# Performance work log

Hardware: AMD Instinct MI355X
Metric: run time of the kernel (lower is better)

Reference implementation:

```python
import jax, jax.numpy as jnp
import numpy as np

N, E, G, H, IN = 200000, 400000, 64, 128, 5
LN_EPS = 1e-5


def setup_inputs() -> dict:
    key = jax.random.key(0)
    ks = jax.random.split(key, 32)
    d = {}
    d["x"] = jax.random.normal(ks[0], (N, IN), jnp.float32)
    d["edge_index"] = jax.random.randint(ks[1], (2, E), 0, N, dtype=jnp.int32)
    d["edge_attr"] = jax.random.normal(ks[2], (E, 1), jnp.float32)
    d["batch"] = jnp.sort(jax.random.randint(ks[3], (N,), 0, G, dtype=jnp.int32))
    dims = [IN, H, H]
    i = 4
    names = [("ew", "eb", "w1_", "b1_", "w2_", "b2_", "g", "bt")]
    for l, din in enumerate(dims):
        d[f"ew{l}"] = jax.random.normal(ks[i], (1, din), jnp.float32); i += 1
        d[f"eb{l}"] = jnp.zeros((din,), jnp.float32)
        d[f"w1_{l}"] = jax.random.normal(ks[i], (din, H), jnp.float32) / np.sqrt(din); i += 1
        d[f"b1_{l}"] = jnp.zeros((H,), jnp.float32)
        d[f"w2_{l}"] = jax.random.normal(ks[i], (H, H), jnp.float32) / np.sqrt(H); i += 1
        d[f"b2_{l}"] = jnp.zeros((H,), jnp.float32)
        d[f"g{l}"] = jnp.ones((H,), jnp.float32)
        d[f"bt{l}"] = jnp.zeros((H,), jnp.float32)
    return d


def _gine_layer(x, src, dst, edge_attr, ew, eb, w1, b1, w2, b2, g, bt):
    # edge encoder: Linear(1, din)
    e = edge_attr @ ew + eb                       # [E, din]
    # GINEConv message: ReLU(x_j + e), aggregated (sum) at destination
    m = jax.nn.relu(x[src] + e)                   # [E, din]
    aggr = jax.ops.segment_sum(m, dst, num_segments=N)  # [N, din]
    h = x + aggr                                  # (1 + eps)*x with eps=0
    # GIN MLP: Linear -> ReLU -> Linear
    h = jax.nn.relu(h @ w1 + b1) @ w2 + b2        # [N, H]
    # LayerNorm
    mu = jnp.mean(h, axis=-1, keepdims=True)
    var = jnp.mean((h - mu) ** 2, axis=-1, keepdims=True)
    h = (h - mu) * jax.lax.rsqrt(var + LN_EPS) * g + bt
    return jax.nn.relu(h)


def reference(x, edge_index, edge_attr, batch,
              ew0, eb0, w1_0, b1_0, w2_0, b2_0, g0, bt0,
              ew1, eb1, w1_1, b1_1, w2_1, b2_1, g1, bt1,
              ew2, eb2, w1_2, b1_2, w2_2, b2_2, g2, bt2):
    src, dst = edge_index[0], edge_index[1]
    x = _gine_layer(x, src, dst, edge_attr, ew0, eb0, w1_0, b1_0, w2_0, b2_0, g0, bt0)
    x = _gine_layer(x, src, dst, edge_attr, ew1, eb1, w1_1, b1_1, w2_1, b2_1, g1, bt1)
    x = _gine_layer(x, src, dst, edge_attr, ew2, eb2, w1_2, b1_2, w2_2, b2_2, g2, bt2)
    # global pooling per graph
    add_pool = jax.ops.segment_sum(x, batch, num_segments=G)           # [G, H]
    counts = jax.ops.segment_sum(jnp.ones((N,), x.dtype), batch, num_segments=G)
    mean_pool = add_pool / jnp.maximum(counts, 1.0)[:, None]           # [G, H]
    return jnp.concatenate([mean_pool, add_pool], axis=1)              # [G, 2H]
```

## Files before the change

### kernel.cpp

```cpp
#include <hip/hip_runtime.h>

#define N_NODES 200000
#define N_EDGES 400000
#define N_GRAPHS 64
#define HDIM 128
#define INDIM 5
#define LN_EPS 1e-5f
#define LDA 140
#define NPBLK 64

typedef __attribute__((ext_vector_type(8))) short short8;
typedef __attribute__((ext_vector_type(4))) float f32x4;
typedef __attribute__((ext_vector_type(2))) float f32x2;

__device__ __forceinline__ unsigned short to_bf(float v) {
    unsigned u = __builtin_bit_cast(unsigned, v);
    return (unsigned short)((u + 0x7FFFu + ((u >> 16) & 1u)) >> 16);
}
__device__ __forceinline__ float bf_lo(unsigned w) { return __builtin_bit_cast(float, w << 16); }
__device__ __forceinline__ float bf_hi(unsigned w) { return __builtin_bit_cast(float, w & 0xFFFF0000u); }
__device__ __forceinline__ float bf2f(unsigned short h) { return __builtin_bit_cast(float, (unsigned)h << 16); }

__device__ __forceinline__ unsigned short cvt1_bf(float v) {
    unsigned r;
    asm("v_cvt_pk_bf16_f32 %0, %1, %1" : "=v"(r) : "v"(v));
    return (unsigned short)r;
}
__device__ __forceinline__ unsigned cvt2_bf(float lo, float hi) {
    unsigned r;
    asm("v_cvt_pk_bf16_f32 %0, %1, %2" : "=v"(r) : "v"(lo), "v"(hi));
    return r;
}
__device__ __forceinline__ f32x2 vmax0(f32x2 v) {
#if __has_builtin(__builtin_elementwise_max)
    return __builtin_elementwise_max(v, (f32x2)0.f);
#else
    v.x = fmaxf(v.x, 0.f);
    v.y = fmaxf(v.y, 0.f);
    return v;
#endif
}

#define GLOAD(p0, p1, p2, p3, srcrow)                                       \
    {                                                                       \
        const uint4* xs_ = (const uint4*)(xin + (size_t)(srcrow)*128 + c0); \
        p0 = xs_[0]; p1 = xs_[1]; p2 = xs_[2]; p3 = xs_[3];                 \
    }

#define GP2(wd, i0)            \
    {                          \
        float4 wb_ = ep[i0];   \
        f32x2 xv_;             \
        xv_.x = bf_lo(wd);     \
        xv_.y = bf_hi(wd);     \
        f32x2 ew_, eb_;        \
        ew_.x = wb_.x;         \
        ew_.y = wb_.y;         \
        eb_.x = wb_.z;         \
        eb_.y = wb_.w;         \
        f32x2 t_ = xv_ + eb_;  \
        t_ = av2_ * ew_ + t_;  \
        accv[i0] += vmax0(t_); \
    }

#define GPROC(p0, p1, p2, p3, a_)                               \
    {                                                           \
        f32x2 av2_;                                             \
        av2_.x = (a_);                                          \
        av2_.y = (a_);                                          \
        GP2(p0.x, 0) GP2(p0.y, 1) GP2(p0.z, 2) GP2(p0.w, 3)     \
        GP2(p1.x, 4) GP2(p1.y, 5) GP2(p1.z, 6) GP2(p1.w, 7)     \
        GP2(p2.x, 8) GP2(p2.y, 9) GP2(p2.z, 10) GP2(p2.w, 11)   \
        GP2(p3.x, 12) GP2(p3.y, 13) GP2(p3.z, 14) GP2(p3.w, 15) \
    }

#define GI2(wd, i0)             \
    {                           \
        accv[i0].x = bf_lo(wd); \
        accv[i0].y = bf_hi(wd); \
    }

#define GINIT(p0, p1, p2, p3)                                   \
    {                                                           \
        GI2(p0.x, 0) GI2(p0.y, 1) GI2(p0.z, 2) GI2(p0.w, 3)     \
        GI2(p1.x, 4) GI2(p1.y, 5) GI2(p1.z, 6) GI2(p1.w, 7)     \
        GI2(p2.x, 8) GI2(p2.y, 9) GI2(p2.z, 10) GI2(p2.w, 11)   \
        GI2(p3.x, 12) GI2(p3.y, 13) GI2(p3.z, 14) GI2(p3.w, 15) \
    }


__global__ void hist_kernel(const int* __restrict__ ei, int* __restrict__ deg) {
    int e = blockIdx.x * blockDim.x + threadIdx.x;
    if (e < N_EDGES) atomicAdd(&deg[ei[N_EDGES + e]], 1);
}

#define SCAN_CHUNK 1024
#define SCAN_BLOCKS ((N_NODES + SCAN_CHUNK - 1) / SCAN_CHUNK)

__global__ __launch_bounds__(256) void scan_phaseA(const int* __restrict__ deg, int* __restrict__ bsums,
                                                   int* __restrict__ poolz) {
    if (blockIdx.x == 0) {
        for (int i = threadIdx.x; i < N_GRAPHS * HDIM + N_GRAPHS; i += 256) poolz[i] = 0;
    }
    __shared__ int red[256];
    int t = threadIdx.x;
    int base = blockIdx.x * SCAN_CHUNK + t * 4;
    int s = 0;
#pragma unroll
    for (int k = 0; k < 4; ++k) {
        int i = base + k;
        s += (i < N_NODES) ? deg[i] : 0;
    }
    red[t] = s;
    __syncthreads();
    for (int off = 128; off; off >>= 1) {
        if (t < off) red[t] += red[t + off];
        __syncthreads();
    }
    if (t == 0) bsums[blockIdx.x] = red[0];
}

__global__ __launch_bounds__(256) void scan_phaseB(int* __restrict__ bsums, int* __restrict__ row_ptr) {
    __shared__ int s[256];
    int t = threadIdx.x;
    int v = (t < SCAN_BLOCKS) ? bsums[t] : 0;
    s[t] = v;
    __syncthreads();
    for (int off = 1; off < 256; off <<= 1) {
        int add = (t >= off) ? s[t - off] : 0;
        __syncthreads();
        s[t] += add;
        __syncthreads();
    }
    if (t < SCAN_BLOCKS) bsums[t] = s[t] - v;
    if (t == SCAN_BLOCKS - 1) row_ptr[N_NODES] = s[t];
}

__global__ __launch_bounds__(256) void scan_phaseC(const int* __restrict__ deg,
                                                   const int* __restrict__ bsums,
                                                   int* __restrict__ row_ptr,
                                                   int* __restrict__ cursor) {
    __shared__ int ts[256];
    int t = threadIdx.x;
    int base = blockIdx.x * SCAN_CHUNK + t * 4;
    int v[4];
    int s = 0;
#pragma unroll
    for (int k = 0; k < 4; ++k) {
        int i = base + k;
        v[k] = (i < N_NODES) ? deg[i] : 0;
        s += v[k];
    }
    ts[t] = s;
    __syncthreads();
    for (int off = 1; off < 256; off <<= 1) {
        int add = (t >= off) ? ts[t - off] : 0;
        __syncthreads();
        ts[t] += add;
        __syncthreads();
    }
    int run = bsums[blockIdx.x] + ts[t] - s;
#pragma unroll
    for (int k = 0; k < 4; ++k) {
        int i = base + k;
        if (i < N_NODES) { row_ptr[i] = run; cursor[i] = 0; }
        run += v[k];
    }
}

#define SCATTER_BLOCKS ((N_EDGES + 255) / 256)

__global__ void scatter_pack(const int* __restrict__ ei, const float* __restrict__ ea,
                             const int* __restrict__ row_ptr, int* __restrict__ cursor,
                             int2* __restrict__ csr,
                             const float* __restrict__ s0, short* __restrict__ d0,
                             const float* __restrict__ s1, short* __restrict__ d1,
                             const float* __restrict__ s2, short* __restrict__ d2,
                             const float* __restrict__ s3, short* __restrict__ d3,
                             const float* __restrict__ s4, short* __restrict__ d4,
                             const float* __restrict__ s5, short* __restrict__ d5) {
    int b = blockIdx.x;
    if (b < SCATTER_BLOCKS) {
        int e = b * 256 + threadIdx.x;
        if (e >= N_EDGES) return;
        int d = ei[N_EDGES + e];
        int pos = atomicAdd(&cursor[d], 1);
        csr[row_ptr[d] + pos] = make_int2(ei[e], __float_as_int(ea[e]));
        return;
    }
    b -= SCATTER_BLOCKS;
    const float* W;
    short* D;
    int din, KP, b0;
    if (b < 16)       { W = s0; D = d0; din = 5;   KP = 32;  b0 = 0; }
    else if (b < 80)  { W = s1; D = d1; din = 128; KP = 128; b0 = 16; }
    else if (b < 144) { W = s2; D = d2; din = 128; KP = 128; b0 = 80; }
    else if (b < 208) { W = s3; D = d3; din = 128; KP = 128; b0 = 144; }
    else if (b < 272) { W = s4; D = d4; din = 128; KP = 128; b0 = 208; }
    else              { W = s5; D = d5; din = 128; KP = 128; b0 = 272; }
    int idx = (b - b0) * 256 + threadIdx.x;
    if (idx >= KP * 128) return;
    int j = idx & 7;
    int lane = (idx >> 3) & 63;
    int rest = idx >> 9;
    int KS = KP >> 5;
    int kstep = rest % KS;
    int tile = rest / KS;
    int k = kstep * 32 + ((lane >> 4) * 8) + j;
    int n = tile * 16 + (lane & 15);
    float v = (k < din) ? W[k * 128 + n] : 0.f;
    D[idx] = (short)to_bf(v);
}

template <int KP1, bool POOL>
__global__ __launch_bounds__(256, 4) void layer_fused(
    const void* __restrict__ xin_v, const int* __restrict__ row_ptr,
    const int2* __restrict__ csr,
    const float* __restrict__ ew, const float* __restrict__ eb,
    const short* __restrict__ w1h, const float* __restrict__ b1,
    const short* __restrict__ w2h, const float* __restrict__ b2,
    const float* __restrict__ g, const float* __restrict__ bt,
    unsigned short* __restrict__ xout,
    const int* __restrict__ batch, float* __restrict__ pool, int* __restrict__ cnt) {
    __shared__ __align__(16) unsigned short A16[NPBLK * LDA];
    __shared__ int bidx[NPBLK];
    union Scratch {
        float4 eweb4[4 * 17];
        float part[KP1 == 128 ? 1 : NPBLK][4][INDIM];
    };
    __shared__ __align__(16) Scratch u;

    int tid = threadIdx.x;
    int node0 = blockIdx.x * NPBLK;

    if constexpr (KP1 == 128) {
        const unsigned short* xin = (const unsigned short*)xin_v;
        if (tid < 64) {
            int qq = tid >> 4, ii = tid & 15, c = qq * 32 + ii * 2;
            u.eweb4[qq * 17 + ii] = make_float4(ew[c], ew[c + 1], eb[c], eb[c + 1]);
        }
        if (POOL && tid >= 64 && tid < 128) bidx[tid - 64] = batch[node0 + tid - 64];

        int row = tid >> 2, qt = tid & 3, c0 = qt * 32;
        int node = node0 + row;

        const uint4* xn = (const uint4*)(xin + (size_t)node * 128 + c0);
        uint4 o0 = xn[0], o1 = xn[1], o2 = xn[2], o3 = xn[3];
        int beg = row_ptr[node], end = row_ptr[node + 1];

        uint4 va0, va1, va2, va3;
        float aA = 0.f;
        int2 rC = make_int2(0, 0), rD = rC;
        if (beg < end) {
            int2 r = csr[beg];
            aA = __int_as_float(r.y);
            GLOAD(va0, va1, va2, va3, r.x);
        }
        if (beg + 1 < end) rC = csr[beg + 1];
        if (beg + 2 < end) rD = csr[beg + 2];
        __syncthreads();
        const float4* ep = u.eweb4 + qt * 17;

        f32x2 accv[16];
        GINIT(o0, o1, o2, o3);

        int e = beg;
        while (e + 1 < end) {
            GPROC(va0, va1, va2, va3, aA);
            aA = __int_as_float(rC.y);
            GLOAD(va0, va1, va2, va3, rC.x);
            rC = rD;
            int i3 = min(e + 3, end - 1);
            rD = csr[i3];
            ++e;
        }
        if (e < end) GPROC(va0, va1, va2, va3, aA);

        uint2* Ar2 = (uint2*)&A16[row * LDA + c0];
#pragma unroll
        for (int k = 0; k < 8; ++k) {
            Ar2[k] = make_uint2(cvt2_bf(accv[2 * k].x, accv[2 * k].y),
                                cvt2_bf(accv[2 * k + 1].x, accv[2 * k + 1].y));
        }
    } else {
        const float* xinf = (const float*)xin_v;
        int row = tid >> 2, qt = tid & 3;
        int node = node0 + row;
        {
            float w[INDIM], b[INDIM], acc[INDIM];
#pragma unroll
            for (int j = 0; j < INDIM; ++j) {
                w[j] = ew[j];
                b[j] = eb[j];
                acc[j] = 0.f;
            }
            int beg = row_ptr[node], end = row_ptr[node + 1];
            int2 r;
            if (beg + qt < end) r = csr[beg + qt];
            for (int e = beg + qt; e < end; e += 4) {
                int2 rn = (e + 4 < end) ? csr[e + 4] : r;
                float a = __int_as_float(r.y);
#pragma unroll
                for (int j = 0; j < INDIM; ++j)
                    acc[j] += fmaxf(fmaf(a, w[j], xinf[r.x * INDIM + j] + b[j]), 0.f);
                r = rn;
            }
#pragma unroll
            for (int j = 0; j < INDIM; ++j) u.part[row][qt][j] = acc[j];
        }
        __syncthreads();
        if (tid < NPBLK) {
#pragma unroll
            for (int j = 0; j < INDIM; ++j) {
                float v = xinf[(node0 + tid) * INDIM + j] + u.part[tid][0][j] + u.part[tid][1][j] +
                          u.part[tid][2][j] + u.part[tid][3][j];
                A16[tid * LDA + j] = cvt1_bf(v);
            }
#pragma unroll
            for (int j = INDIM; j < 32; ++j) A16[tid * LDA + j] = 0;
        }
        __syncthreads();
    }

    int wv = tid >> 6, lane = tid & 63;
    int mrow = lane & 15, q = lane >> 4;
    int arow = wv * 16 + mrow;

    const short8* w1p = (const short8*)w1h;
    const short8* w2p = (const short8*)w2h;

    f32x4 acc2[8];
#pragma unroll
    for (int t = 0; t < 8; ++t) acc2[t] = (f32x4){0.f, 0.f, 0.f, 0.f};
    constexpr int KS1 = KP1 / 32;
#pragma unroll
    for (int ks = 0; ks < KS1; ++ks) {
        short8 bh[8];
#pragma unroll
        for (int t = 0; t < 8; ++t) bh[t] = w1p[((size_t)t * KS1 + ks) * 64 + lane];
        short8 ah = *(const short8*)&A16[arow * LDA + ks * 32 + q * 8];
#pragma unroll
        for (int t = 0; t < 8; ++t)
            acc2[t] = __builtin_amdgcn_mfma_f32_16x16x32_bf16(ah, bh[t], acc2[t], 0, 0, 0);
    }
    {
        float b1v[8];
#pragma unroll
        for (int t = 0; t < 8; ++t) b1v[t] = b1[t * 16 + mrow];
#pragma unroll
        for (int t = 0; t < 8; ++t)
#pragma unroll
            for (int r = 0; r < 4; ++r) {
                int rrow = wv * 16 + q * 4 + r;
                int col = t * 16 + mrow;
                A16[rrow * LDA + col] = cvt1_bf(fmaxf(acc2[t][r] + b1v[t], 0.f));
            }
    }

#pragma unroll
    for (int t = 0; t < 8; ++t) acc2[t] = (f32x4){0.f, 0.f, 0.f, 0.f};
#pragma unroll
    for (int ks = 0; ks < 4; ++ks) {
        short8 bh[8];
#pragma unroll
        for (int t = 0; t < 8; ++t) bh[t] = w2p[((size_t)t * 4 + ks) * 64 + lane];
        short8 ah = *(const short8*)&A16[arow * LDA + ks * 32 + q * 8];
#pragma unroll
        for (int t = 0; t < 8; ++t)
            acc2[t] = __builtin_amdgcn_mfma_f32_16x16x32_bf16(ah, bh[t], acc2[t], 0, 0, 0);
    }

    float s4[4] = {0.f, 0.f, 0.f, 0.f}, q4[4] = {0.f, 0.f, 0.f, 0.f};
    {
        float b2v[8];
#pragma unroll
        for (int t = 0; t < 8; ++t) b2v[t] = b2[t * 16 + mrow];
#pragma unroll
        for (int t = 0; t < 8; ++t)
#pragma unroll
            for (int r = 0; r < 4; ++r) {
                float v = acc2[t][r] + b2v[t];
                acc2[t][r] = v;
                s4[r] += v;
                q4[r] += v * v;
            }
    }
#pragma unroll
    for (int m = 1; m <= 8; m <<= 1) {
#pragma unroll
        for (int r = 0; r < 4; ++r) {
            s4[r] += __shfl_xor(s4[r], m, 64);
            q4[r] += __shfl_xor(q4[r], m, 64);
        }
    }
    float mu[4], inv[4];
#pragma unroll
    for (int r = 0; r < 4; ++r) {
        mu[r] = s4[r] * (1.f / HDIM);
        float var = q4[r] * (1.f / HDIM) - mu[r] * mu[r];
        inv[r] = rsqrtf(var + LN_EPS);
    }
    float gv[8], btv[8];
#pragma unroll
    for (int t = 0; t < 8; ++t) {
        gv[t] = g[t * 16 + mrow];
        btv[t] = bt[t * 16 + mrow];
    }

#pragma unroll
    for (int t = 0; t < 8; ++t)
#pragma unroll
        for (int r = 0; r < 4; ++r) {
            int rrow = wv * 16 + q * 4 + r;
            int col = t * 16 + mrow;
            float o = fmaxf((acc2[t][r] - mu[r]) * inv[r] * gv[t] + btv[t], 0.f);
            A16[rrow * LDA + col] = cvt1_bf(o);
        }
    __syncthreads();

    if (!POOL) {
        unsigned* xo = (unsigned*)xout;
#pragma unroll
        for (int i = 0; i < 16; ++i) {
            int idx = tid + 256 * i;
            int row = idx >> 6, w = idx & 63;
            xo[(size_t)(node0 + row) * 64 + w] = ((const unsigned*)&A16[row * LDA])[w];
        }
    } else {
        if (tid < 128) {
            int col = tid;
            float accp = 0.f;
            int cur = bidx[0];
            for (int r = 0; r < NPBLK; ++r) {
                int gi = bidx[r];
                if (gi != cur) {
                    unsafeAtomicAdd(&pool[cur * HDIM + col], accp);
                    accp = 0.f;
                    cur = gi;
                }
                accp += bf2f(A16[r * LDA + col]);
            }
            unsafeAtomicAdd(&pool[cur * HDIM + col], accp);
        } else if (tid == 255) {
            int cur = bidx[0], c = 0;
            for (int r = 0; r < NPBLK; ++r) {
                if (bidx[r] != cur) {
                    atomicAdd(&cnt[cur], c);
                    c = 0;
                    cur = bidx[r];
                }
                ++c;
            }
            atomicAdd(&cnt[cur], c);
        }
    }
}

__global__ void pool_final(const float* __restrict__ pool, const int* __restrict__ cnt,
                           float* __restrict__ out) {
    int g = blockIdx.x, j = threadIdx.x;
    float add = pool[g * HDIM + j];
    float c = (float)max(cnt[g], 1);
    out[g * (2 * HDIM) + j] = add / c;
    out[g * (2 * HDIM) + HDIM + j] = add;
}

extern "C" void kernel_launch(void* const* d_in, const int* in_sizes, int n_in,
                              void* d_out, int out_size, void* d_ws, size_t ws_size,
                              hipStream_t stream) {
    const float* x_in = (const float*)d_in[0];
    const int* ei = (const int*)d_in[1];
    const float* ea = (const float*)d_in[2];
    const int* batch = (const int*)d_in[3];
    const float* P[24];
    for (int i = 0; i < 24; ++i) P[i] = (const float*)d_in[4 + i];

    unsigned short* x_a = (unsigned short*)d_ws;
    unsigned short* x_b = x_a + (size_t)N_NODES * HDIM;
    float* pool = (float*)(x_b + (size_t)N_NODES * HDIM);
    int* cnt = (int*)(pool + N_GRAPHS * HDIM);
    int* deg = cnt + N_GRAPHS;
    int* cursor = deg + N_NODES;
    int* row_ptr = cursor + N_NODES;
    int* bsums = row_ptr + N_NODES + 1;
    int2* csr = (int2*)(bsums + 256);
    short* wp = (short*)(((uintptr_t)(csr + N_EDGES) + 15) & ~(uintptr_t)15);
    float* out = (float*)d_out;

    short *w1h[3], *w2h[3];
    for (int l = 0; l < 3; ++l) {
        w1h[l] = wp + (size_t)l * 32768;
        w2h[l] = w1h[l] + 16384;
    }

    hipMemsetAsync(deg, 0, N_NODES * sizeof(int), stream);

    hist_kernel<<<(N_EDGES + 255) / 256, 256, 0, stream>>>(ei, deg);
    scan_phaseA<<<SCAN_BLOCKS, 256, 0, stream>>>(deg, bsums, (int*)pool);
    scan_phaseB<<<1, 256, 0, stream>>>(bsums, row_ptr);
    scan_phaseC<<<SCAN_BLOCKS, 256, 0, stream>>>(deg, bsums, row_ptr, cursor);

    scatter_pack<<<SCATTER_BLOCKS + 336, 256, 0, stream>>>(
        ei, ea, row_ptr, cursor, csr,
        P[2], w1h[0], P[4], w2h[0],
        P[10], w1h[1], P[12], w2h[1],
        P[18], w1h[2], P[20], w2h[2]);

    layer_fused<32, false><<<N_NODES / NPBLK, 256, 0, stream>>>(
        x_in, row_ptr, csr, P[0], P[1],
        w1h[0], P[3], w2h[0], P[5], P[6], P[7], x_a, nullptr, nullptr, nullptr);
    layer_fused<128, false><<<N_NODES / NPBLK, 256, 0, stream>>>(
        x_a, row_ptr, csr, P[8], P[9],
        w1h[1], P[11], w2h[1], P[13], P[14], P[15], x_b, nullptr, nullptr, nullptr);
    layer_fused<128, true><<<N_NODES / NPBLK, 256, 0, stream>>>(
        x_b, row_ptr, csr, P[16], P[17],
        w1h[2], P[19], w2h[2], P[21], P[22], P[23], nullptr, batch, pool, cnt);

    pool_final<<<N_GRAPHS, HDIM, 0, stream>>>(pool, cnt, out);
}
```

Measured before the change: 344.2 us.

## Double nodes per block to 128 with two MFMA row tiles per wave

```diff
diff --git a/kernel.cpp b/kernel.cpp
--- a/kernel.cpp
+++ b/kernel.cpp
@@ -7,7 +7,8 @@
 #define INDIM 5
 #define LN_EPS 1e-5f
 #define LDA 140
-#define NPBLK 64
+#define NPBLK 128
+#define NBLKS ((N_NODES + NPBLK - 1) / NPBLK)
 
 typedef __attribute__((ext_vector_type(8))) short short8;
 typedef __attribute__((ext_vector_type(4))) float f32x4;
@@ -41,10 +42,11 @@
 #endif
 }
 
-#define GLOAD(p0, p1, p2, p3, srcrow)                                       \
+#define GLOAD8(y0, y1, y2, y3, y4, y5, y6, y7, srcrow)                      \
     {                                                                       \
         const uint4* xs_ = (const uint4*)(xin + (size_t)(srcrow)*128 + c0); \
-        p0 = xs_[0]; p1 = xs_[1]; p2 = xs_[2]; p3 = xs_[3];                 \
+        y0 = xs_[0]; y1 = xs_[1]; y2 = xs_[2]; y3 = xs_[3];                 \
+        y4 = xs_[4]; y5 = xs_[5]; y6 = xs_[6]; y7 = xs_[7];                 \
     }
 
 #define GP2(wd, i0)            \
@@ -63,15 +65,19 @@
         accv[i0] += vmax0(t_); \
     }
 
-#define GPROC(p0, p1, p2, p3, a_)                               \
+#define GPROC8(y0, y1, y2, y3, y4, y5, y6, y7, a_)              \
     {                                                           \
         f32x2 av2_;                                             \
         av2_.x = (a_);                                          \
         av2_.y = (a_);                                          \
-        GP2(p0.x, 0) GP2(p0.y, 1) GP2(p0.z, 2) GP2(p0.w, 3)     \
-        GP2(p1.x, 4) GP2(p1.y, 5) GP2(p1.z, 6) GP2(p1.w, 7)     \
-        GP2(p2.x, 8) GP2(p2.y, 9) GP2(p2.z, 10) GP2(p2.w, 11)   \
-        GP2(p3.x, 12) GP2(p3.y, 13) GP2(p3.z, 14) GP2(p3.w, 15) \
+        GP2(y0.x, 0) GP2(y0.y, 1) GP2(y0.z, 2) GP2(y0.w, 3)     \
+        GP2(y1.x, 4) GP2(y1.y, 5) GP2(y1.z, 6) GP2(y1.w, 7)     \
+        GP2(y2.x, 8) GP2(y2.y, 9) GP2(y2.z, 10) GP2(y2.w, 11)   \
+        GP2(y3.x, 12) GP2(y3.y, 13) GP2(y3.z, 14) GP2(y3.w, 15) \
+        GP2(y4.x, 16) GP2(y4.y, 17) GP2(y4.z, 18) GP2(y4.w, 19) \
+        GP2(y5.x, 20) GP2(y5.y, 21) GP2(y5.z, 22) GP2(y5.w, 23) \
+        GP2(y6.x, 24) GP2(y6.y, 25) GP2(y6.z, 26) GP2(y6.w, 27) \
+        GP2(y7.x, 28) GP2(y7.y, 29) GP2(y7.z, 30) GP2(y7.w, 31) \
     }
 
 #define GI2(wd, i0)             \
@@ -80,12 +86,16 @@
         accv[i0].y = bf_hi(wd); \
     }
 
-#define GINIT(p0, p1, p2, p3)                                   \
+#define GINIT8(y0, y1, y2, y3, y4, y5, y6, y7)                  \
     {                                                           \
-        GI2(p0.x, 0) GI2(p0.y, 1) GI2(p0.z, 2) GI2(p0.w, 3)     \
-        GI2(p1.x, 4) GI2(p1.y, 5) GI2(p1.z, 6) GI2(p1.w, 7)     \
-        GI2(p2.x, 8) GI2(p2.y, 9) GI2(p2.z, 10) GI2(p2.w, 11)   \
-        GI2(p3.x, 12) GI2(p3.y, 13) GI2(p3.z, 14) GI2(p3.w, 15) \
+        GI2(y0.x, 0) GI2(y0.y, 1) GI2(y0.z, 2) GI2(y0.w, 3)     \
+        GI2(y1.x, 4) GI2(y1.y, 5) GI2(y1.z, 6) GI2(y1.w, 7)     \
+        GI2(y2.x, 8) GI2(y2.y, 9) GI2(y2.z, 10) GI2(y2.w, 11)   \
+        GI2(y3.x, 12) GI2(y3.y, 13) GI2(y3.z, 14) GI2(y3.w, 15) \
+        GI2(y4.x, 16) GI2(y4.y, 17) GI2(y4.z, 18) GI2(y4.w, 19) \
+        GI2(y5.x, 20) GI2(y5.y, 21) GI2(y5.z, 22) GI2(y5.w, 23) \
+        GI2(y6.x, 24) GI2(y6.y, 25) GI2(y6.z, 26) GI2(y6.w, 27) \
+        GI2(y7.x, 28) GI2(y7.y, 29) GI2(y7.z, 30) GI2(y7.w, 31) \
     }
 
 
@@ -225,8 +235,8 @@
     __shared__ __align__(16) unsigned short A16[NPBLK * LDA];
     __shared__ int bidx[NPBLK];
     union Scratch {
-        float4 eweb4[4 * 17];
-        float part[KP1 == 128 ? 1 : NPBLK][4][INDIM];
+        float4 eweb4[2 * 33];
+        float part[KP1 == 128 ? 1 : NPBLK][2][INDIM];
     };
     __shared__ __align__(16) Scratch u;
 
@@ -236,56 +246,57 @@
     if constexpr (KP1 == 128) {
         const unsigned short* xin = (const unsigned short*)xin_v;
         if (tid < 64) {
-            int qq = tid >> 4, ii = tid & 15, c = qq * 32 + ii * 2;
-            u.eweb4[qq * 17 + ii] = make_float4(ew[c], ew[c + 1], eb[c], eb[c + 1]);
-        }
-        if (POOL && tid >= 64 && tid < 128) bidx[tid - 64] = batch[node0 + tid - 64];
-
-        int row = tid >> 2, qt = tid & 3, c0 = qt * 32;
-        int node = node0 + row;
+            int hh = tid >> 5, ii = tid & 31, c = hh * 64 + ii * 2;
+            u.eweb4[hh * 33 + ii] = make_float4(ew[c], ew[c + 1], eb[c], eb[c + 1]);
+        }
+        if (POOL && tid >= 128) bidx[tid - 128] = batch[min(node0 + tid - 128, N_NODES - 1)];
+
+        int row = tid >> 1, half = tid & 1, c0 = half * 64;
+        int node = min(node0 + row, N_NODES - 1);
 
         const uint4* xn = (const uint4*)(xin + (size_t)node * 128 + c0);
         uint4 o0 = xn[0], o1 = xn[1], o2 = xn[2], o3 = xn[3];
+        uint4 o4 = xn[4], o5 = xn[5], o6 = xn[6], o7 = xn[7];
         int beg = row_ptr[node], end = row_ptr[node + 1];
 
-        uint4 va0, va1, va2, va3;
+        uint4 va0, va1, va2, va3, va4, va5, va6, va7;
         float aA = 0.f;
         int2 rC = make_int2(0, 0), rD = rC;
         if (beg < end) {
             int2 r = csr[beg];
             aA = __int_as_float(r.y);
-            GLOAD(va0, va1, va2, va3, r.x);
+            GLOAD8(va0, va1, va2, va3, va4, va5, va6, va7, r.x);
         }
         if (beg + 1 < end) rC = csr[beg + 1];
         if (beg + 2 < end) rD = csr[beg + 2];
         __syncthreads();
-        const float4* ep = u.eweb4 + qt * 17;
-
-        f32x2 accv[16];
-        GINIT(o0, o1, o2, o3);
+        const float4* ep = u.eweb4 + half * 33;
+
+        f32x2 accv[32];
+        GINIT8(o0, o1, o2, o3, o4, o5, o6, o7);
 
         int e = beg;
         while (e + 1 < end) {
-            GPROC(va0, va1, va2, va3, aA);
+            GPROC8(va0, va1, va2, va3, va4, va5, va6, va7, aA);
             aA = __int_as_float(rC.y);
-            GLOAD(va0, va1, va2, va3, rC.x);
+            GLOAD8(va0, va1, va2, va3, va4, va5, va6, va7, rC.x);
             rC = rD;
             int i3 = min(e + 3, end - 1);
             rD = csr[i3];
             ++e;
         }
-        if (e < end) GPROC(va0, va1, va2, va3, aA);
+        if (e < end) GPROC8(va0, va1, va2, va3, va4, va5, va6, va7, aA);
 
         uint2* Ar2 = (uint2*)&A16[row * LDA + c0];
 #pragma unroll
-        for (int k = 0; k < 8; ++k) {
+        for (int k = 0; k < 16; ++k) {
             Ar2[k] = make_uint2(cvt2_bf(accv[2 * k].x, accv[2 * k].y),
                                 cvt2_bf(accv[2 * k + 1].x, accv[2 * k + 1].y));
         }
     } else {
         const float* xinf = (const float*)xin_v;
-        int row = tid >> 2, qt = tid & 3;
-        int node = node0 + row;
+        int row = tid >> 1, qt = tid & 1;
+        int node = min(node0 + row, N_NODES - 1);
         {
             float w[INDIM], b[INDIM], acc[INDIM];
 #pragma unroll
@@ -297,8 +308,8 @@
             int beg = row_ptr[node], end = row_ptr[node + 1];
             int2 r;
             if (beg + qt < end) r = csr[beg + qt];
-            for (int e = beg + qt; e < end; e += 4) {
-                int2 rn = (e + 4 < end) ? csr[e + 4] : r;
+            for (int e = beg + qt; e < end; e += 2) {
+                int2 rn = (e + 2 < end) ? csr[e + 2] : r;
                 float a = __int_as_float(r.y);
 #pragma unroll
                 for (int j = 0; j < INDIM; ++j)
@@ -310,10 +321,10 @@
         }
         __syncthreads();
         if (tid < NPBLK) {
+            int nd = min(node0 + tid, N_NODES - 1);
 #pragma unroll
             for (int j = 0; j < INDIM; ++j) {
-                float v = xinf[(node0 + tid) * INDIM + j] + u.part[tid][0][j] + u.part[tid][1][j] +
-                          u.part[tid][2][j] + u.part[tid][3][j];
+                float v = xinf[nd * INDIM + j] + u.part[tid][0][j] + u.part[tid][1][j];
                 A16[tid * LDA + j] = cvt1_bf(v);
             }
 #pragma unroll
@@ -324,82 +335,105 @@
 
     int wv = tid >> 6, lane = tid & 63;
     int mrow = lane & 15, q = lane >> 4;
-    int arow = wv * 16 + mrow;
+    int ar0 = wv * 32 + mrow;
+    int ar1 = wv * 32 + 16 + mrow;
 
     const short8* w1p = (const short8*)w1h;
     const short8* w2p = (const short8*)w2h;
 
-    f32x4 acc2[8];
-#pragma unroll
-    for (int t = 0; t < 8; ++t) acc2[t] = (f32x4){0.f, 0.f, 0.f, 0.f};
+    f32x4 acc2[2][8];
+#pragma unroll
+    for (int gg = 0; gg < 2; ++gg)
+#pragma unroll
+        for (int t = 0; t < 8; ++t) acc2[gg][t] = (f32x4){0.f, 0.f, 0.f, 0.f};
     constexpr int KS1 = KP1 / 32;
 #pragma unroll
     for (int ks = 0; ks < KS1; ++ks) {
         short8 bh[8];
 #pragma unroll
         for (int t = 0; t < 8; ++t) bh[t] = w1p[((size_t)t * KS1 + ks) * 64 + lane];
-        short8 ah = *(const short8*)&A16[arow * LDA + ks * 32 + q * 8];
-#pragma unroll
-        for (int t = 0; t < 8; ++t)
-            acc2[t] = __builtin_amdgcn_mfma_f32_16x16x32_bf16(ah, bh[t], acc2[t], 0, 0, 0);
+        short8 ah0 = *(const short8*)&A16[ar0 * LDA + ks * 32 + q * 8];
+        short8 ah1 = *(const short8*)&A16[ar1 * LDA + ks * 32 + q * 8];
+#pragma unroll
+        for (int t = 0; t < 8; ++t) {
+            acc2[0][t] = __builtin_amdgcn_mfma_f32_16x16x32_bf16(ah0, bh[t], acc2[0][t], 0, 0, 0);
+            acc2[1][t] = __builtin_amdgcn_mfma_f32_16x16x32_bf16(ah1, bh[t], acc2[1][t], 0, 0, 0);
+        }
     }
     {
         float b1v[8];
 #pragma unroll
         for (int t = 0; t < 8; ++t) b1v[t] = b1[t * 16 + mrow];
 #pragma unroll
-        for (int t = 0; t < 8; ++t)
-#pragma unroll
-            for (int r = 0; r < 4; ++r) {
-                int rrow = wv * 16 + q * 4 + r;
-                int col = t * 16 + mrow;
-                A16[rrow * LDA + col] = cvt1_bf(fmaxf(acc2[t][r] + b1v[t], 0.f));
-            }
-    }
-
-#pragma unroll
-    for (int t = 0; t < 8; ++t) acc2[t] = (f32x4){0.f, 0.f, 0.f, 0.f};
+        for (int gg = 0; gg < 2; ++gg)
+#pragma unroll
+            for (int t = 0; t < 8; ++t)
+#pragma unroll
+                for (int r = 0; r < 4; ++r) {
+                    int rrow = wv * 32 + gg * 16 + q * 4 + r;
+                    int col = t * 16 + mrow;
+                    A16[rrow * LDA + col] = cvt1_bf(fmaxf(acc2[gg][t][r] + b1v[t], 0.f));
+                }
+    }
+
+#pragma unroll
+    for (int gg = 0; gg < 2; ++gg)
+#pragma unroll
+        for (int t = 0; t < 8; ++t) acc2[gg][t] = (f32x4){0.f, 0.f, 0.f, 0.f};
 #pragma unroll
     for (int ks = 0; ks < 4; ++ks) {
         short8 bh[8];
 #pragma unroll
         for (int t = 0; t < 8; ++t) bh[t] = w2p[((size_t)t * 4 + ks) * 64 + lane];
-        short8 ah = *(const short8*)&A16[arow * LDA + ks * 32 + q * 8];
-#pragma unroll
-        for (int t = 0; t < 8; ++t)
-            acc2[t] = __builtin_amdgcn_mfma_f32_16x16x32_bf16(ah, bh[t], acc2[t], 0, 0, 0);
-    }
-
-    float s4[4] = {0.f, 0.f, 0.f, 0.f}, q4[4] = {0.f, 0.f, 0.f, 0.f};
+        short8 ah0 = *(const short8*)&A16[ar0 * LDA + ks * 32 + q * 8];
+        short8 ah1 = *(const short8*)&A16[ar1 * LDA + ks * 32 + q * 8];
+#pragma unroll
+        for (int t = 0; t < 8; ++t) {
+            acc2[0][t] = __builtin_amdgcn_mfma_f32_16x16x32_bf16(ah0, bh[t], acc2[0][t], 0, 0, 0);
+            acc2[1][t] = __builtin_amdgcn_mfma_f32_16x16x32_bf16(ah1, bh[t], acc2[1][t], 0, 0, 0);
+        }
+    }
+
+    float s4[2][4], q4[2][4];
+#pragma unroll
+    for (int gg = 0; gg < 2; ++gg)
+#pragma unroll
+        for (int r = 0; r < 4; ++r) { s4[gg][r] = 0.f; q4[gg][r] = 0.f; }
     {
         float b2v[8];
 #pragma unroll
         for (int t = 0; t < 8; ++t) b2v[t] = b2[t * 16 + mrow];
 #pragma unroll
-        for (int t = 0; t < 8; ++t)
+        for (int gg = 0; gg < 2; ++gg)
+#pragma unroll
+            for (int t = 0; t < 8; ++t)
+#pragma unroll
+                for (int r = 0; r < 4; ++r) {
+                    float v = acc2[gg][t][r] + b2v[t];
+                    acc2[gg][t][r] = v;
+                    s4[gg][r] += v;
+                    q4[gg][r] += v * v;
+                }
+    }
+#pragma unroll
+    for (int m = 1; m <= 8; m <<= 1) {
+#pragma unroll
+        for (int gg = 0; gg < 2; ++gg)
 #pragma unroll
             for (int r = 0; r < 4; ++r) {
-                float v = acc2[t][r] + b2v[t];
-                acc2[t][r] = v;
-                s4[r] += v;
-                q4[r] += v * v;
-            }
-    }
-#pragma unroll
-    for (int m = 1; m <= 8; m <<= 1) {
+                s4[gg][r] += __shfl_xor(s4[gg][r], m, 64);
+                q4[gg][r] += __shfl_xor(q4[gg][r], m, 64);
+            }
+    }
+    float mu[2][4], inv[2][4];
+#pragma unroll
+    for (int gg = 0; gg < 2; ++gg)
 #pragma unroll
         for (int r = 0; r < 4; ++r) {
-            s4[r] += __shfl_xor(s4[r], m, 64);
-            q4[r] += __shfl_xor(q4[r], m, 64);
-        }
-    }
-    float mu[4], inv[4];
-#pragma unroll
-    for (int r = 0; r < 4; ++r) {
-        mu[r] = s4[r] * (1.f / HDIM);
-        float var = q4[r] * (1.f / HDIM) - mu[r] * mu[r];
-        inv[r] = rsqrtf(var + LN_EPS);
-    }
+            mu[gg][r] = s4[gg][r] * (1.f / HDIM);
+            float var = q4[gg][r] * (1.f / HDIM) - mu[gg][r] * mu[gg][r];
+            inv[gg][r] = rsqrtf(var + LN_EPS);
+        }
     float gv[8], btv[8];
 #pragma unroll
     for (int t = 0; t < 8; ++t) {
@@ -408,30 +442,34 @@
     }
 
 #pragma unroll
-    for (int t = 0; t < 8; ++t)
-#pragma unroll
-        for (int r = 0; r < 4; ++r) {
-            int rrow = wv * 16 + q * 4 + r;
-            int col = t * 16 + mrow;
-            float o = fmaxf((acc2[t][r] - mu[r]) * inv[r] * gv[t] + btv[t], 0.f);
-            A16[rrow * LDA + col] = cvt1_bf(o);
-        }
+    for (int gg = 0; gg < 2; ++gg)
+#pragma unroll
+        for (int t = 0; t < 8; ++t)
+#pragma unroll
+            for (int r = 0; r < 4; ++r) {
+                int rrow = wv * 32 + gg * 16 + q * 4 + r;
+                int col = t * 16 + mrow;
+                float o = fmaxf((acc2[gg][t][r] - mu[gg][r]) * inv[gg][r] * gv[t] + btv[t], 0.f);
+                A16[rrow * LDA + col] = cvt1_bf(o);
+            }
     __syncthreads();
 
     if (!POOL) {
         unsigned* xo = (unsigned*)xout;
 #pragma unroll
-        for (int i = 0; i < 16; ++i) {
+        for (int i = 0; i < 32; ++i) {
             int idx = tid + 256 * i;
             int row = idx >> 6, w = idx & 63;
-            xo[(size_t)(node0 + row) * 64 + w] = ((const unsigned*)&A16[row * LDA])[w];
+            if (node0 + row < N_NODES)
+                xo[(size_t)(node0 + row) * 64 + w] = ((const unsigned*)&A16[row * LDA])[w];
         }
     } else {
+        int rmax = min(NPBLK, N_NODES - node0);
         if (tid < 128) {
             int col = tid;
             float accp = 0.f;
             int cur = bidx[0];
-            for (int r = 0; r < NPBLK; ++r) {
+            for (int r = 0; r < rmax; ++r) {
                 int gi = bidx[r];
                 if (gi != cur) {
                     unsafeAtomicAdd(&pool[cur * HDIM + col], accp);
@@ -443,7 +481,7 @@
             unsafeAtomicAdd(&pool[cur * HDIM + col], accp);
         } else if (tid == 255) {
             int cur = bidx[0], c = 0;
-            for (int r = 0; r < NPBLK; ++r) {
+            for (int r = 0; r < rmax; ++r) {
                 if (bidx[r] != cur) {
                     atomicAdd(&cnt[cur], c);
                     c = 0;
@@ -506,13 +544,13 @@
         P[10], w1h[1], P[12], w2h[1],
         P[18], w1h[2], P[20], w2h[2]);
 
-    layer_fused<32, false><<<N_NODES / NPBLK, 256, 0, stream>>>(
+    layer_fused<32, false><<<NBLKS, 256, 0, stream>>>(
         x_in, row_ptr, csr, P[0], P[1],
         w1h[0], P[3], w2h[0], P[5], P[6], P[7], x_a, nullptr, nullptr, nullptr);
-    layer_fused<128, false><<<N_NODES / NPBLK, 256, 0, stream>>>(
+    layer_fused<128, false><<<NBLKS, 256, 0, stream>>>(
         x_a, row_ptr, csr, P[8], P[9],
         w1h[1], P[11], w2h[1], P[13], P[14], P[15], x_b, nullptr, nullptr, nullptr);
-    layer_fused<128, true><<<N_NODES / NPBLK, 256, 0, stream>>>(
+    layer_fused<128, true><<<NBLKS, 256, 0, stream>>>(
         x_b, row_ptr, csr, P[16], P[17],
         w1h[2], P[19], w2h[2], P[21], P[22], P[23], nullptr, batch, pool, cnt);
 
```

Result: slower. 668.4 us (+94.2%).

## Reorder nodes by in-degree within each graph to balance aggregation work

Applied to the files above, without the earlier changes.

```diff
diff --git a/kernel.cpp b/kernel.cpp
--- a/kernel.cpp
+++ b/kernel.cpp
@@ -94,6 +94,58 @@
     if (e < N_EDGES) atomicAdd(&deg[ei[N_EDGES + e]], 1);
 }
 
+__global__ void gbounds(const int* __restrict__ batch, int* __restrict__ gbnd) {
+    int g = threadIdx.x;
+    if (g > N_GRAPHS) return;
+    int lo = 0, hi = N_NODES;
+    while (lo < hi) {
+        int mid = (lo + hi) >> 1;
+        if (batch[mid] < g) lo = mid + 1;
+        else hi = mid;
+    }
+    gbnd[g] = lo;
+}
+
+__global__ __launch_bounds__(256) void gsort(const int* __restrict__ deg,
+                                             const int* __restrict__ gbnd,
+                                             int* __restrict__ perm, int* __restrict__ iperm) {
+    __shared__ int bins[64], offs[64];
+    int g = blockIdx.x;
+    int s = gbnd[g], e2 = gbnd[g + 1];
+    int t = threadIdx.x;
+    if (t < 64) bins[t] = 0;
+    __syncthreads();
+    for (int i = s + t; i < e2; i += 256) atomicAdd(&bins[min(deg[i], 63)], 1);
+    __syncthreads();
+    if (t == 0) {
+        int run = 0;
+        for (int b = 0; b < 64; ++b) { offs[b] = run; run += bins[b]; }
+    }
+    __syncthreads();
+    if (t < 64) bins[t] = 0;
+    __syncthreads();
+    for (int i = s + t; i < e2; i += 256) {
+        int b = min(deg[i], 63);
+        int r = atomicAdd(&bins[b], 1);
+        int pos = s + offs[b] + r;
+        perm[pos] = i;
+        iperm[i] = pos;
+    }
+}
+
+__global__ void permute_kernel(const int* __restrict__ perm, const int* __restrict__ deg,
+                               const int* __restrict__ batch, const float* __restrict__ x_in,
+                               int* __restrict__ degp, int* __restrict__ batchp,
+                               float* __restrict__ xp) {
+    int p = blockIdx.x * 256 + threadIdx.x;
+    if (p >= N_NODES) return;
+    int o = perm[p];
+    degp[p] = deg[o];
+    batchp[p] = batch[o];
+#pragma unroll
+    for (int j = 0; j < INDIM; ++j) xp[p * INDIM + j] = x_in[o * INDIM + j];
+}
+
 #define SCAN_CHUNK 1024
 #define SCAN_BLOCKS ((N_NODES + SCAN_CHUNK - 1) / SCAN_CHUNK)
 
@@ -172,7 +224,7 @@
 
 __global__ void scatter_pack(const int* __restrict__ ei, const float* __restrict__ ea,
                              const int* __restrict__ row_ptr, int* __restrict__ cursor,
-                             int2* __restrict__ csr,
+                             int2* __restrict__ csr, const int* __restrict__ iperm,
                              const float* __restrict__ s0, short* __restrict__ d0,
                              const float* __restrict__ s1, short* __restrict__ d1,
                              const float* __restrict__ s2, short* __restrict__ d2,
@@ -183,9 +235,10 @@
     if (b < SCATTER_BLOCKS) {
         int e = b * 256 + threadIdx.x;
         if (e >= N_EDGES) return;
-        int d = ei[N_EDGES + e];
+        int d = iperm[ei[N_EDGES + e]];
+        int src = iperm[ei[e]];
         int pos = atomicAdd(&cursor[d], 1);
-        csr[row_ptr[d] + pos] = make_int2(ei[e], __float_as_int(ea[e]));
+        csr[row_ptr[d] + pos] = make_int2(src, __float_as_int(ea[e]));
         return;
     }
     b -= SCATTER_BLOCKS;
@@ -483,7 +536,13 @@
     int* cursor = deg + N_NODES;
     int* row_ptr = cursor + N_NODES;
     int* bsums = row_ptr + N_NODES + 1;
-    int2* csr = (int2*)(bsums + 256);
+    int* gbnd = bsums + 256;
+    int* perm = gbnd + 128;
+    int* iperm = perm + N_NODES;
+    int* degp = iperm + N_NODES;
+    int* batchp = degp + N_NODES;
+    float* xp = (float*)(batchp + N_NODES);
+    int2* csr = (int2*)(((uintptr_t)(xp + (size_t)N_NODES * INDIM) + 15) & ~(uintptr_t)15);
     short* wp = (short*)(((uintptr_t)(csr + N_EDGES) + 15) & ~(uintptr_t)15);
     float* out = (float*)d_out;
 
@@ -496,25 +555,30 @@
     hipMemsetAsync(deg, 0, N_NODES * sizeof(int), stream);
 
     hist_kernel<<<(N_EDGES + 255) / 256, 256, 0, stream>>>(ei, deg);
-    scan_phaseA<<<SCAN_BLOCKS, 256, 0, stream>>>(deg, bsums, (int*)pool);
+    gbounds<<<1, 128, 0, stream>>>(batch, gbnd);
+    gsort<<<N_GRAPHS, 256, 0, stream>>>(deg, gbnd, perm, iperm);
+    permute_kernel<<<(N_NODES + 255) / 256, 256, 0, stream>>>(perm, deg, batch, x_in,
+                                                              degp, batchp, xp);
+
+    scan_phaseA<<<SCAN_BLOCKS, 256, 0, stream>>>(degp, bsums, (int*)pool);
     scan_phaseB<<<1, 256, 0, stream>>>(bsums, row_ptr);
-    scan_phaseC<<<SCAN_BLOCKS, 256, 0, stream>>>(deg, bsums, row_ptr, cursor);
+    scan_phaseC<<<SCAN_BLOCKS, 256, 0, stream>>>(degp, bsums, row_ptr, cursor);
 
     scatter_pack<<<SCATTER_BLOCKS + 336, 256, 0, stream>>>(
-        ei, ea, row_ptr, cursor, csr,
+        ei, ea, row_ptr, cursor, csr, iperm,
         P[2], w1h[0], P[4], w2h[0],
         P[10], w1h[1], P[12], w2h[1],
         P[18], w1h[2], P[20], w2h[2]);
 
     layer_fused<32, false><<<N_NODES / NPBLK, 256, 0, stream>>>(
-        x_in, row_ptr, csr, P[0], P[1],
+        xp, row_ptr, csr, P[0], P[1],
         w1h[0], P[3], w2h[0], P[5], P[6], P[7], x_a, nullptr, nullptr, nullptr);
     layer_fused<128, false><<<N_NODES / NPBLK, 256, 0, stream>>>(
         x_a, row_ptr, csr, P[8], P[9],
         w1h[1], P[11], w2h[1], P[13], P[14], P[15], x_b, nullptr, nullptr, nullptr);
     layer_fused<128, true><<<N_NODES / NPBLK, 256, 0, stream>>>(
         x_b, row_ptr, csr, P[16], P[17],
-        w1h[2], P[19], w2h[2], P[21], P[22], P[23], nullptr, batch, pool, cnt);
+        w1h[2], P[19], w2h[2], P[21], P[22], P[23], nullptr, batchp, pool, cnt);
 
     pool_final<<<N_GRAPHS, HDIM, 0, stream>>>(pool, cnt, out);
 }
```

Measured after the change: 343.8 us. No clear change (-0.1%).

## Reorder nodes by in-degree within each graph to balance gather work

Applied to the files above, without the earlier changes.

```diff
diff --git a/kernel.cpp b/kernel.cpp
--- a/kernel.cpp
+++ b/kernel.cpp
@@ -92,6 +92,43 @@
 __global__ void hist_kernel(const int* __restrict__ ei, int* __restrict__ deg) {
     int e = blockIdx.x * blockDim.x + threadIdx.x;
     if (e < N_EDGES) atomicAdd(&deg[ei[N_EDGES + e]], 1);
+}
+
+__global__ void gbounds(const int* __restrict__ batch, int* __restrict__ gbnd) {
+    int g = threadIdx.x;
+    if (g > N_GRAPHS) return;
+    int lo = 0, hi = N_NODES;
+    while (lo < hi) {
+        int mid = (lo + hi) >> 1;
+        if (batch[mid] < g) lo = mid + 1;
+        else hi = mid;
+    }
+    gbnd[g] = lo;
+}
+
+__global__ __launch_bounds__(256) void gsort(const int* __restrict__ deg,
+                                             const int* __restrict__ gbnd,
+                                             int* __restrict__ perm) {
+    __shared__ int bins[64], offs[64];
+    int g = blockIdx.x;
+    int s = gbnd[g], e2 = gbnd[g + 1];
+    int t = threadIdx.x;
+    if (t < 64) bins[t] = 0;
+    __syncthreads();
+    for (int i = s + t; i < e2; i += 256) atomicAdd(&bins[min(deg[i], 63)], 1);
+    __syncthreads();
+    if (t == 0) {
+        int run = 0;
+        for (int b = 0; b < 64; ++b) { offs[b] = run; run += bins[b]; }
+    }
+    __syncthreads();
+    if (t < 64) bins[t] = 0;
+    __syncthreads();
+    for (int i = s + t; i < e2; i += 256) {
+        int b = min(deg[i], 63);
+        int r = atomicAdd(&bins[b], 1);
+        perm[s + offs[b] + r] = i;
+    }
 }
 
 #define SCAN_CHUNK 1024
@@ -215,7 +252,7 @@
 template <int KP1, bool POOL>
 __global__ __launch_bounds__(256, 4) void layer_fused(
     const void* __restrict__ xin_v, const int* __restrict__ row_ptr,
-    const int2* __restrict__ csr,
+    const int2* __restrict__ csr, const int* __restrict__ perm,
     const float* __restrict__ ew, const float* __restrict__ eb,
     const short* __restrict__ w1h, const float* __restrict__ b1,
     const short* __restrict__ w2h, const float* __restrict__ b2,
@@ -224,6 +261,7 @@
     const int* __restrict__ batch, float* __restrict__ pool, int* __restrict__ cnt) {
     __shared__ __align__(16) unsigned short A16[NPBLK * LDA];
     __shared__ int bidx[NPBLK];
+    __shared__ int pidx[NPBLK];
     union Scratch {
         float4 eweb4[4 * 17];
         float part[KP1 == 128 ? 1 : NPBLK][4][INDIM];
@@ -233,20 +271,22 @@
     int tid = threadIdx.x;
     int node0 = blockIdx.x * NPBLK;
 
+    if (tid >= 128 && tid < 192) pidx[tid - 128] = perm[node0 + tid - 128];
+
     if constexpr (KP1 == 128) {
         const unsigned short* xin = (const unsigned short*)xin_v;
         if (tid < 64) {
             int qq = tid >> 4, ii = tid & 15, c = qq * 32 + ii * 2;
             u.eweb4[qq * 17 + ii] = make_float4(ew[c], ew[c + 1], eb[c], eb[c + 1]);
         }
-        if (POOL && tid >= 64 && tid < 128) bidx[tid - 64] = batch[node0 + tid - 64];
+        if (POOL && tid >= 64 && tid < 128) bidx[tid - 64] = batch[perm[node0 + tid - 64]];
 
         int row = tid >> 2, qt = tid & 3, c0 = qt * 32;
-        int node = node0 + row;
-
-        const uint4* xn = (const uint4*)(xin + (size_t)node * 128 + c0);
+        int prow = perm[node0 + row];
+
+        const uint4* xn = (const uint4*)(xin + (size_t)prow * 128 + c0);
         uint4 o0 = xn[0], o1 = xn[1], o2 = xn[2], o3 = xn[3];
-        int beg = row_ptr[node], end = row_ptr[node + 1];
+        int beg = row_ptr[prow], end = row_ptr[prow + 1];
 
         uint4 va0, va1, va2, va3;
         float aA = 0.f;
@@ -285,7 +325,7 @@
     } else {
         const float* xinf = (const float*)xin_v;
         int row = tid >> 2, qt = tid & 3;
-        int node = node0 + row;
+        int prow = perm[node0 + row];
         {
             float w[INDIM], b[INDIM], acc[INDIM];
 #pragma unroll
@@ -294,7 +334,7 @@
                 b[j] = eb[j];
                 acc[j] = 0.f;
             }
-            int beg = row_ptr[node], end = row_ptr[node + 1];
+            int beg = row_ptr[prow], end = row_ptr[prow + 1];
             int2 r;
             if (beg + qt < end) r = csr[beg + qt];
             for (int e = beg + qt; e < end; e += 4) {
@@ -312,7 +352,7 @@
         if (tid < NPBLK) {
 #pragma unroll
             for (int j = 0; j < INDIM; ++j) {
-                float v = xinf[(node0 + tid) * INDIM + j] + u.part[tid][0][j] + u.part[tid][1][j] +
+                float v = xinf[pidx[tid] * INDIM + j] + u.part[tid][0][j] + u.part[tid][1][j] +
                           u.part[tid][2][j] + u.part[tid][3][j];
                 A16[tid * LDA + j] = cvt1_bf(v);
             }
@@ -424,7 +464,7 @@
         for (int i = 0; i < 16; ++i) {
             int idx = tid + 256 * i;
             int row = idx >> 6, w = idx & 63;
-            xo[(size_t)(node0 + row) * 64 + w] = ((const unsigned*)&A16[row * LDA])[w];
+            xo[(size_t)pidx[row] * 64 + w] = ((const unsigned*)&A16[row * LDA])[w];
         }
     } else {
         if (tid < 128) {
@@ -483,7 +523,9 @@
     int* cursor = deg + N_NODES;
     int* row_ptr = cursor + N_NODES;
     int* bsums = row_ptr + N_NODES + 1;
-    int2* csr = (int2*)(bsums + 256);
+    int* gbnd = bsums + 256;
+    int* perm = gbnd + 128;
+    int2* csr = (int2*)(((uintptr_t)(perm + N_NODES) + 15) & ~(uintptr_t)15);
     short* wp = (short*)(((uintptr_t)(csr + N_EDGES) + 15) & ~(uintptr_t)15);
     float* out = (float*)d_out;
 
@@ -496,6 +538,9 @@
     hipMemsetAsync(deg, 0, N_NODES * sizeof(int), stream);
 
     hist_kernel<<<(N_EDGES + 255) / 256, 256, 0, stream>>>(ei, deg);
+    gbounds<<<1, 128, 0, stream>>>(batch, gbnd);
+    gsort<<<N_GRAPHS, 256, 0, stream>>>(deg, gbnd, perm);
+
     scan_phaseA<<<SCAN_BLOCKS, 256, 0, stream>>>(deg, bsums, (int*)pool);
     scan_phaseB<<<1, 256, 0, stream>>>(bsums, row_ptr);
     scan_phaseC<<<SCAN_BLOCKS, 256, 0, stream>>>(deg, bsums, row_ptr, cursor);
@@ -507,13 +552,13 @@
         P[18], w1h[2], P[20], w2h[2]);
 
     layer_fused<32, false><<<N_NODES / NPBLK, 256, 0, stream>>>(
-        x_in, row_ptr, csr, P[0], P[1],
+        x_in, row_ptr, csr, perm, P[0], P[1],
         w1h[0], P[3], w2h[0], P[5], P[6], P[7], x_a, nullptr, nullptr, nullptr);
     layer_fused<128, false><<<N_NODES / NPBLK, 256, 0, stream>>>(
-        x_a, row_ptr, csr, P[8], P[9],
+        x_a, row_ptr, csr, perm, P[8], P[9],
         w1h[1], P[11], w2h[1], P[13], P[14], P[15], x_b, nullptr, nullptr, nullptr);
     layer_fused<128, true><<<N_NODES / NPBLK, 256, 0, stream>>>(
-        x_b, row_ptr, csr, P[16], P[17],
+        x_b, row_ptr, csr, perm, P[16], P[17],
         w1h[2], P[19], w2h[2], P[21], P[22], P[23], nullptr, batch, pool, cnt);
 
     pool_final<<<N_GRAPHS, HDIM, 0, stream>>>(pool, cnt, out);
```

After: 344.5 us. No clear change (+0.1%).
